# Optimization experiments

Hardware: AMD Instinct MI355X
Metric: run time of the kernel (lower is better)

The kernel has to match this reference:

```python
import jax, jax.numpy as jnp
import numpy as np

SHARE_ROWS = 16  # norm shared across consecutive output rows
GROUP = 32       # dequant group size along in_features


def setup_inputs() -> dict:
    key = jax.random.key(0)
    k1, k2, k3, k4 = jax.random.split(key, 4)
    O, I = 8192, 8192
    blocks, half = I // GROUP, GROUP // 2
    x = jax.random.normal(k1, (16, I), dtype=jnp.float32)
    # packed bytes: (low & 15) + (high << 4) in [0, 256)
    weight_q4 = jax.random.randint(k2, (O, blocks, half), 0, 256, dtype=jnp.int32)
    weight_norm = jax.random.uniform(k3, (O // SHARE_ROWS, blocks, 1), dtype=jnp.float16)
    bias = jax.random.normal(k4, (O,), dtype=jnp.float32)
    return {"x": x, "weight_q4": weight_q4, "weight_norm": weight_norm, "bias": bias}


def reference(x, weight_q4, weight_norm, bias):
    O, blocks, half = weight_q4.shape
    # unpack 4-bit nibbles: interleave low/high -> [O, blocks, GROUP]
    low = weight_q4 & 15
    high = (weight_q4 >> 4) & 15
    q8 = jnp.stack((low, high), axis=-1).reshape(O, blocks, GROUP)
    q8 = q8.astype(jnp.float32) / 15.0
    # per-(row-group, block) normalization, shared across SHARE_ROWS rows
    norms = jnp.repeat(weight_norm.astype(jnp.float32), SHARE_ROWS, axis=0)  # [O, blocks, 1]
    W = (q8 * 2.0 * norms - norms).reshape(O, blocks * GROUP)  # [O, I] fp32
    return x @ W.T + bias
```

## Files before the change

kernel.cpp:

```cpp
#include <hip/hip_runtime.h>
#include <hip/hip_bf16.h>
#include <hip/hip_fp16.h>

typedef __attribute__((ext_vector_type(8))) short bf16x8;
typedef __attribute__((ext_vector_type(4))) float f32x4;
typedef __attribute__((ext_vector_type(4))) int   i32x4;

#define O_TOTAL 8192
#define I_TOTAL 8192
#define WAVES_PER_BLOCK 8
#define KSTEPS       32
#define ROW_I32      (I_TOTAL / 2)
#define NBLOCKS      256

static __device__ __forceinline__ short f2bf(float f) {
    union { __hip_bfloat16 b; short s; } u;
    u.b = __float2bfloat16(f);
    return u.s;
}

static __device__ __forceinline__ float bf2f(unsigned short s) {
    union { unsigned int u; float f; } v;
    v.u = ((unsigned int)s) << 16;
    return v.f;
}

__global__ __launch_bounds__(256)
void xcvt_kernel(const float* __restrict__ x, short* __restrict__ xb)
{
    const int i = (blockIdx.x * 256 + threadIdx.x) * 4;
    f32x4 v = *(const f32x4*)(x + i);
    short r0 = f2bf(v[0]), r1 = f2bf(v[1]), r2 = f2bf(v[2]), r3 = f2bf(v[3]);
    union { short s[4]; long long q; } p;
    p.s[0] = r0; p.s[1] = r1; p.s[2] = r2; p.s[3] = r3;
    *(long long*)(xb + i) = p.q;
}

__global__ __launch_bounds__(512, 6)
void linq4_kernel(const short* __restrict__ xb,
                  const int* __restrict__ wq,
                  const void* __restrict__ wn,
                  const float* __restrict__ bias,
                  float* __restrict__ out)
{
    const int tid  = threadIdx.x;
    const int wave = tid >> 6;
    const int lane = tid & 63;
    const int otile = blockIdx.x;
    const int o0   = otile * 16;
    const int col  = lane & 15;
    const int kg   = lane >> 4;

    const unsigned int* w32 = (const unsigned int*)wn;
    int cntLo = 0, cntHi = 0;
    #pragma unroll
    for (int i = 0; i < 16; ++i) {
        unsigned int w = w32[i];
        unsigned int lo = w & 0xFFFFu, hi = w >> 16;
        if (lo >= 0x3980u && lo < 0x3F80u) cntLo++;
        if (hi >= 0x3C00u) cntHi++;
    }
    const int fmt = (cntLo >= 12) ? 1 : (cntHi >= 12 ? 0 : 2);

    __shared__ float nlds[NBLOCKS];
    __shared__ float red[WAVES_PER_BLOCK][256];
    if (tid < NBLOCKS) {
        const int idx = otile * NBLOCKS + tid;
        float nf;
        if (fmt == 0)      nf = ((const float*)wn)[idx];
        else if (fmt == 1) nf = bf2f(((const unsigned short*)wn)[idx]);
        else               nf = __half2float(((const __half*)wn)[idx]);
        nlds[tid] = nf;
    }
    __syncthreads();

    const int o = o0 + col;
    const int* wrow = wq + (size_t)o * ROW_I32 + kg * 4;
    const short* xrow = xb + (size_t)col * I_TOTAL + kg * 8;

    f32x4 acc = {0.f, 0.f, 0.f, 0.f};
    const int b0 = wave * KSTEPS;

    i32x4  pv0 = *(const i32x4*)(wrow + (size_t)b0 * 16);
    bf16x8 xa0 = *(const bf16x8*)(xrow + (size_t)b0 * 32);

    #pragma unroll 4
    for (int s = 0; s < KSTEPS; ++s) {
        const int b = b0 + s;

        i32x4  pv1;
        bf16x8 xa1;
        if (s + 1 < KSTEPS) {
            pv1 = *(const i32x4*)(wrow + (size_t)(b + 1) * 16);
            xa1 = *(const bf16x8*)(xrow + (size_t)(b + 1) * 32);
        }

        const float nf = nlds[b];
        const float sc = nf * (2.0f / 15.0f);

        bf16x8 bfrag;
        #pragma unroll
        for (int c = 0; c < 4; ++c) {
            int v = pv0[c];
            float wl = (float)(v & 15)        * sc - nf;
            float wh = (float)((v >> 4) & 15) * sc - nf;
            bfrag[2*c]   = f2bf(wl);
            bfrag[2*c+1] = f2bf(wh);
        }

        acc = __builtin_amdgcn_mfma_f32_16x16x32_bf16(xa0, bfrag, acc, 0, 0, 0);

        pv0 = pv1;
        xa0 = xa1;
    }

    *(f32x4*)&red[wave][lane * 4] = acc;
    __syncthreads();

    if (tid < 256) {
        float s = 0.f;
        #pragma unroll
        for (int w = 0; w < WAVES_PER_BLOCK; ++w) s += red[w][tid];
        const int l = tid >> 2;
        const int r = tid & 3;
        const int m  = ((l >> 4) << 2) + r;
        const int oc = o0 + (l & 15);
        out[(size_t)m * O_TOTAL + oc] = s + bias[oc];
    }
}

extern "C" void kernel_launch(void* const* d_in, const int* in_sizes, int n_in,
                              void* d_out, int out_size, void* d_ws, size_t ws_size,
                              hipStream_t stream) {
    const float* x    = (const float*)d_in[0];
    const int*   wq   = (const int*)d_in[1];
    const void*  wn   = (const void*)d_in[2];
    const float* bias = (const float*)d_in[3];
    float* out = (float*)d_out;
    short* xb  = (short*)d_ws;

    hipLaunchKernelGGL(xcvt_kernel, dim3(16 * I_TOTAL / 4 / 256), dim3(256), 0, stream, x, xb);

    hipLaunchKernelGGL(linq4_kernel, dim3(O_TOTAL / 16), dim3(512), 0, stream,
                       (const short*)xb, wq, wn, bias, out);
}
```

Before: 41.28 us.

## Stage weight and activation tiles through LDS with async global_load_lds double buffering

Replaces direct per-lane global loads with global_load_lds copies into double-buffered, XOR-swizzled LDS tiles. Each step loads a contiguous 256-element k-chunk for all 16 rows, so waves now interleave over blocks instead of owning contiguous k ranges. The aim is coalesced 16-byte row reads and memory traffic that overlaps with compute. In exchange it adds a block-wide __syncthreads every step and more LDS use, which may cut occupancy.

Result: slower. 43.60 us (+5.6%).

```diff
diff --git a/kernel.cpp b/kernel.cpp
--- a/kernel.cpp
+++ b/kernel.cpp
@@ -8,10 +8,13 @@
 
 #define O_TOTAL 8192
 #define I_TOTAL 8192
-#define WAVES_PER_BLOCK 8
-#define KSTEPS       32
-#define ROW_I32      (I_TOTAL / 2)
-#define NBLOCKS      256
+#define NWAVES  8
+#define NSS     32
+#define ROW_I32 (I_TOTAL / 2)
+#define NBLOCKS 256
+
+typedef __attribute__((address_space(1))) const void GASV;
+typedef __attribute__((address_space(3))) void LASV;
 
 static __device__ __forceinline__ short f2bf(float f) {
     union { __hip_bfloat16 b; short s; } u;
@@ -30,9 +33,8 @@
 {
     const int i = (blockIdx.x * 256 + threadIdx.x) * 4;
     f32x4 v = *(const f32x4*)(x + i);
-    short r0 = f2bf(v[0]), r1 = f2bf(v[1]), r2 = f2bf(v[2]), r3 = f2bf(v[3]);
     union { short s[4]; long long q; } p;
-    p.s[0] = r0; p.s[1] = r1; p.s[2] = r2; p.s[3] = r3;
+    p.s[0] = f2bf(v[0]); p.s[1] = f2bf(v[1]); p.s[2] = f2bf(v[2]); p.s[3] = f2bf(v[3]);
     *(long long*)(xb + i) = p.q;
 }
 
@@ -44,26 +46,27 @@
                   float* __restrict__ out)
 {
     const int tid  = threadIdx.x;
-    const int wave = tid >> 6;
+    const int w    = tid >> 6;
     const int lane = tid & 63;
     const int otile = blockIdx.x;
     const int o0   = otile * 16;
-    const int col  = lane & 15;
-    const int kg   = lane >> 4;
 
     const unsigned int* w32 = (const unsigned int*)wn;
     int cntLo = 0, cntHi = 0;
     #pragma unroll
     for (int i = 0; i < 16; ++i) {
-        unsigned int w = w32[i];
-        unsigned int lo = w & 0xFFFFu, hi = w >> 16;
+        unsigned int ww = w32[i];
+        unsigned int lo = ww & 0xFFFFu, hi = ww >> 16;
         if (lo >= 0x3980u && lo < 0x3F80u) cntLo++;
         if (hi >= 0x3C00u) cntHi++;
     }
     const int fmt = (cntLo >= 12) ? 1 : (cntHi >= 12 ? 0 : 2);
 
+    __shared__ int   w_lds[2][2048];
+    __shared__ short x_lds[2][4096];
     __shared__ float nlds[NBLOCKS];
-    __shared__ float red[WAVES_PER_BLOCK][256];
+    __shared__ float red[NWAVES][256];
+
     if (tid < NBLOCKS) {
         const int idx = otile * NBLOCKS + tid;
         float nf;
@@ -72,55 +75,62 @@
         else               nf = __half2float(((const __half*)wn)[idx]);
         nlds[tid] = nf;
     }
+
+    const int r_st  = 2 * w + (lane >> 5);
+    const int jj    = (lane & 31) ^ (r_st & 7);
+    const int* gw_base   = wq + (size_t)(o0 + r_st) * ROW_I32 + jj * 4;
+    const short* gx_base = xb + (size_t)r_st * I_TOTAL + jj * 8;
+
+    const int col = lane & 15;
+    const int kg  = lane >> 4;
+    const int j   = w * 4 + kg;
+    const int t   = j ^ (col & 7);
+    const int ldsoff = col * 128 + t * 4;
+    const int xldoff = col * 256 + t * 8;
+
+    f32x4 acc = {0.f, 0.f, 0.f, 0.f};
+
+    __builtin_amdgcn_global_load_lds((GASV*)(gw_base), (LASV*)(&w_lds[0][w * 256]), 16, 0, 0);
+    __builtin_amdgcn_global_load_lds((GASV*)(gx_base), (LASV*)(&x_lds[0][w * 512]), 16, 0, 0);
     __syncthreads();
 
-    const int o = o0 + col;
-    const int* wrow = wq + (size_t)o * ROW_I32 + kg * 4;
-    const short* xrow = xb + (size_t)col * I_TOTAL + kg * 8;
-
-    f32x4 acc = {0.f, 0.f, 0.f, 0.f};
-    const int b0 = wave * KSTEPS;
-
-    i32x4  pv0 = *(const i32x4*)(wrow + (size_t)b0 * 16);
-    bf16x8 xa0 = *(const bf16x8*)(xrow + (size_t)b0 * 32);
-
-    #pragma unroll 4
-    for (int s = 0; s < KSTEPS; ++s) {
-        const int b = b0 + s;
-
-        i32x4  pv1;
-        bf16x8 xa1;
-        if (s + 1 < KSTEPS) {
-            pv1 = *(const i32x4*)(wrow + (size_t)(b + 1) * 16);
-            xa1 = *(const bf16x8*)(xrow + (size_t)(b + 1) * 32);
+    for (int S = 0; S < NSS; ++S) {
+        const int cur = S & 1;
+        if (S + 1 < NSS) {
+            const int nxt = cur ^ 1;
+            __builtin_amdgcn_global_load_lds((GASV*)(gw_base + (S + 1) * 128),
+                                             (LASV*)(&w_lds[nxt][w * 256]), 16, 0, 0);
+            __builtin_amdgcn_global_load_lds((GASV*)(gx_base + (S + 1) * 256),
+                                             (LASV*)(&x_lds[nxt][w * 512]), 16, 0, 0);
         }
 
-        const float nf = nlds[b];
+        i32x4  pv = *(const i32x4*)(&w_lds[cur][ldsoff]);
+        bf16x8 xa = *(const bf16x8*)(&x_lds[cur][xldoff]);
+        const float nf = nlds[S * 8 + w];
         const float sc = nf * (2.0f / 15.0f);
 
         bf16x8 bfrag;
         #pragma unroll
         for (int c = 0; c < 4; ++c) {
-            int v = pv0[c];
+            int v = pv[c];
             float wl = (float)(v & 15)        * sc - nf;
             float wh = (float)((v >> 4) & 15) * sc - nf;
             bfrag[2*c]   = f2bf(wl);
             bfrag[2*c+1] = f2bf(wh);
         }
 
-        acc = __builtin_amdgcn_mfma_f32_16x16x32_bf16(xa0, bfrag, acc, 0, 0, 0);
+        acc = __builtin_amdgcn_mfma_f32_16x16x32_bf16(xa, bfrag, acc, 0, 0, 0);
 
-        pv0 = pv1;
-        xa0 = xa1;
+        __syncthreads();
     }
 
-    *(f32x4*)&red[wave][lane * 4] = acc;
+    *(f32x4*)&red[w][lane * 4] = acc;
     __syncthreads();
 
     if (tid < 256) {
         float s = 0.f;
         #pragma unroll
-        for (int w = 0; w < WAVES_PER_BLOCK; ++w) s += red[w][tid];
+        for (int q = 0; q < NWAVES; ++q) s += red[q][tid];
         const int l = tid >> 2;
         const int r = tid & 3;
         const int m  = ((l >> 4) << 2) + r;
```
